# Kernel tuning notes

Hardware: AMD Instinct MI355X
Metric: run time of the kernel (lower is better)

## Reference

```python
import jax, jax.numpy as jnp
import numpy as np

N = 100000      # nodes
E = 3200000     # edges (avg degree 32)
F_IN = 16       # node_feature_size
R1, R2, R3 = 8, 16, 8   # gcn hidden sizes
N1 = 32                  # mlp hidden


def _lin(k, fan_in, shape):
    s = 1.0 / np.sqrt(fan_in)
    return jax.random.uniform(k, shape, minval=-s, maxval=s, dtype=jnp.float32)


def setup_inputs() -> dict:
    key = jax.random.key(0)
    ks = jax.random.split(key, 16)
    x = jax.random.normal(ks[0], (N, F_IN), dtype=jnp.float32)
    edge_index = jax.random.randint(ks[1], (2, E), 0, N, dtype=jnp.int64)
    return {
        "x": x,
        "edge_index": edge_index,
        # GraphConv k: out = mean_agg(x_j) @ W_rel + b + x @ W_root  (PyG GraphConv, lin_root bias=False)
        "W_rel1": _lin(ks[2], F_IN, (F_IN, R1)), "b1": _lin(ks[3], F_IN, (R1,)), "W_root1": _lin(ks[4], F_IN, (F_IN, R1)),
        "W_rel2": _lin(ks[5], R1, (R1, R2)),   "b2": _lin(ks[6], R1, (R2,)),   "W_root2": _lin(ks[7], R1, (R1, R2)),
        "W_rel3": _lin(ks[8], R2, (R2, R3)),   "b3": _lin(ks[9], R2, (R3,)),   "W_root3": _lin(ks[10], R2, (R2, R3)),
        "fc1_W": _lin(ks[11], R3, (R3, N1)), "fc1_b": _lin(ks[12], R3, (N1,)),
        "fc2_W": _lin(ks[13], N1, (N1, 1)),  "fc2_b": _lin(ks[14], N1, (1,)),
    }


def _graph_conv(x, src, dst, W_rel, b, W_root):
    # message: gather source features; aggregate: mean over incoming edges at dst
    n = x.shape[0]
    msg_sum = jax.ops.segment_sum(x[src], dst, num_segments=n)          # [N, F]
    cnt = jax.ops.segment_sum(jnp.ones(src.shape, x.dtype), dst, num_segments=n)
    mean = msg_sum / jnp.maximum(cnt, 1.0)[:, None]
    return mean @ W_rel + b + x @ W_root


def reference(x, edge_index, W_rel1, b1, W_root1, W_rel2, b2, W_root2,
              W_rel3, b3, W_root3, fc1_W, fc1_b, fc2_W, fc2_b):
    src, dst = edge_index[0], edge_index[1]
    h = jax.nn.sigmoid(_graph_conv(x, src, dst, W_rel1, b1, W_root1))
    h = jax.nn.sigmoid(_graph_conv(h, src, dst, W_rel2, b2, W_root2))
    h = jax.nn.sigmoid(_graph_conv(h, src, dst, W_rel3, b3, W_root3))
    h = jax.nn.sigmoid(h @ fc1_W + fc1_b)
    return h @ fc2_W + fc2_b   # [N, 1]
```

## Files before the change

kernel.cpp:

```cpp
#include <hip/hip_runtime.h>
#include <math.h>


#define CHUNK  8192
#define PSTR   10752
#define BW     128
#define MAXB   6144
#define MAXNB  800
#define MAXBLK 512

typedef _Float16 half8 __attribute__((ext_vector_type(8)));

static __device__ __forceinline__ float sigmoidf_(float x) {
    return 1.0f / (1.0f + expf(-x));
}

static __device__ __forceinline__ int scan256_excl(int v, int* s) {
    int tid = threadIdx.x;
    s[tid] = v;
    for (int off = 1; off < 256; off <<= 1) {
        __syncthreads();
        int t = (tid >= off) ? s[tid - off] : 0;
        __syncthreads();
        s[tid] += t;
    }
    __syncthreads();
    return s[tid] - v;
}

static __device__ __forceinline__ void gather_mean8(
    const half8* __restrict__ t, const int* __restrict__ csr,
    int rs, int d, float* s) {
#pragma unroll
    for (int c = 0; c < 8; ++c) s[c] = 0.0f;
    int e = 0;
    for (; e + 4 <= d; e += 4) {
        int4 ci = *(const int4*)(csr + rs + e);
        half8 v0 = t[ci.x]; half8 v1 = t[ci.y];
        half8 v2 = t[ci.z]; half8 v3 = t[ci.w];
#pragma unroll
        for (int c = 0; c < 8; ++c)
            s[c] += ((float)v0[c] + (float)v1[c]) + ((float)v2[c] + (float)v3[c]);
    }
    for (; e < d; ++e) {
        half8 v = t[csr[rs + e]];
#pragma unroll
        for (int c = 0; c < 8; ++c) s[c] += (float)v[c];
    }
    float inv = 1.0f / (float)(d > 0 ? d : 1);
#pragma unroll
    for (int c = 0; c < 8; ++c) s[c] *= inv;
}

__global__ __launch_bounds__(256)
void bin_sort_kernel(const float* __restrict__ x, const float* __restrict__ W1r,
                     const float* __restrict__ b1v, const float* __restrict__ W1o,
                     _Float16* __restrict__ t1, _Float16* __restrict__ z1,
                     const int* __restrict__ src, const int* __restrict__ dst,
                     unsigned* __restrict__ packed, int* __restrict__ counts_bm,
                     int* __restrict__ lstart_bm, int* __restrict__ btot,
                     int E, int N, int NB, int NBLK) {
    __shared__ int s_hist[MAXNB];
    __shared__ int s_cur[MAXNB];
    __shared__ unsigned s_pk[PSTR];
    __shared__ int s_scan[256];
    __shared__ float sW[264];
    int tid = threadIdx.x, blk = blockIdx.x;

    if (tid < 128) { sW[tid] = W1r[tid]; sW[128 + tid] = W1o[tid]; }
    if (tid < 8) sW[256 + tid] = b1v[tid];
    for (int i = tid; i < NB; i += 256) s_hist[i] = 0;
    __syncthreads();
    {
        int node = blk * 256 + tid;
        if (node < N) {
            const float4* x4 = (const float4*)x;
            float xv[16];
#pragma unroll
            for (int k = 0; k < 4; ++k) {
                float4 v = x4[node * 4 + k];
                xv[4 * k] = v.x; xv[4 * k + 1] = v.y;
                xv[4 * k + 2] = v.z; xv[4 * k + 3] = v.w;
            }
            float ta[8], za[8];
#pragma unroll
            for (int j = 0; j < 8; ++j) { ta[j] = 0.0f; za[j] = sW[256 + j]; }
#pragma unroll
            for (int f = 0; f < 16; ++f) {
                float xf = xv[f];
#pragma unroll
                for (int j = 0; j < 8; ++j) {
                    ta[j] += xf * sW[f * 8 + j];
                    za[j] += xf * sW[128 + f * 8 + j];
                }
            }
            half8 th, zh;
#pragma unroll
            for (int j = 0; j < 8; ++j) { th[j] = (_Float16)ta[j]; zh[j] = (_Float16)za[j]; }
            ((half8*)t1)[node] = th;
            ((half8*)z1)[node] = zh;
        }
    }

    if (blk >= NBLK) return;

    int base = blk * CHUNK;
    int cnt = E - base; if (cnt > CHUNK) cnt = CHUNK;

    if (cnt == CHUNK) {
        const int4* d4 = (const int4*)(dst + base);
#pragma unroll
        for (int k = 0; k < CHUNK / 1024; ++k) {
            int4 d = d4[k * 256 + tid];
            atomicAdd(&s_hist[d.x >> 7], 1);
            atomicAdd(&s_hist[d.y >> 7], 1);
            atomicAdd(&s_hist[d.z >> 7], 1);
            atomicAdd(&s_hist[d.w >> 7], 1);
        }
    } else {
        for (int i = tid; i < cnt; i += 256) atomicAdd(&s_hist[dst[base + i] >> 7], 1);
    }
    __syncthreads();

    int per = (NB + 255) / 256;
    int st = tid * per;
    int lsum = 0;
    for (int j = 0; j < per; ++j)
        if (st + j < NB) lsum += (s_hist[st + j] + 3) & ~3;
    int excl = scan256_excl(lsum, s_scan);
    int padtot = s_scan[255];
    int run = excl;
    for (int j = 0; j < per; ++j)
        if (st + j < NB) { s_cur[st + j] = run; run += (s_hist[st + j] + 3) & ~3; }
    __syncthreads();

    if (cnt == CHUNK) {
        const int4* d4 = (const int4*)(dst + base);
        const int4* s4 = (const int4*)(src + base);
#pragma unroll
        for (int k = 0; k < CHUNK / 1024; ++k) {
            int4 d = d4[k * 256 + tid];
            int4 s = s4[k * 256 + tid];
            int dd[4] = {d.x, d.y, d.z, d.w};
            int ss[4] = {s.x, s.y, s.z, s.w};
#pragma unroll
            for (int j = 0; j < 4; ++j) {
                int pos = atomicAdd(&s_cur[dd[j] >> 7], 1);
                s_pk[pos] = ((unsigned)(dd[j] & 127) << 17) | (unsigned)ss[j];
            }
        }
    } else {
        for (int i = tid; i < cnt; i += 256) {
            int d = dst[base + i], s = src[base + i];
            int pos = atomicAdd(&s_cur[d >> 7], 1);
            s_pk[pos] = ((unsigned)(d & 127) << 17) | (unsigned)s;
        }
    }
    __syncthreads();

    for (int i = tid; i < padtot; i += 256) packed[(size_t)blk * PSTR + i] = s_pk[i];
    for (int i = tid; i < NB; i += 256) {
        int h = s_hist[i];
        counts_bm[blk * NB + i] = h;
        lstart_bm[blk * NB + i] = s_cur[i] - h;
        if (h) atomicAdd(&btot[i], h);
    }
}

__global__ __launch_bounds__(256)
void bucket_sort_kernel(const unsigned* __restrict__ packed,
                        const int* __restrict__ counts_bm,
                        const int* __restrict__ lstart_bm,
                        const int* __restrict__ btot,
                        int* __restrict__ csr_src, int* __restrict__ deg,
                        int* __restrict__ rowstart, int N, int NB, int NBLK) {
    __shared__ int s_cnt[MAXBLK], s_lst[MAXBLK], s_off[MAXBLK];
    __shared__ unsigned s_p[MAXB];
    __shared__ int s_out[MAXB];
    __shared__ int h[BW], hs[BW], curb[BW];
    __shared__ int s_scan[256];
    __shared__ int s_tot, s_ptot;
    int b = blockIdx.x, tid = threadIdx.x;

    int partial = 0;
    for (int i = tid; i < b; i += 256) partial += ((btot[i] + 3) & ~3) + 512;
    scan256_excl(partial, s_scan);
    int beg = s_scan[255];

    for (int i = tid; i < NBLK; i += 256) {
        s_cnt[i] = counts_bm[i * NB + b];
        s_lst[i] = lstart_bm[i * NB + b];
    }
    __syncthreads();

    int per = (NBLK + 255) / 256;
    int st = tid * per;
    int lsum = 0;
    for (int j = 0; j < per; ++j)
        if (st + j < NBLK) lsum += s_cnt[st + j];
    int excl = scan256_excl(lsum, s_scan);
    if (tid == 255) s_tot = s_scan[255];
    int run = excl;
    for (int j = 0; j < per; ++j)
        if (st + j < NBLK) { s_off[st + j] = run; run += s_cnt[st + j]; }
    __syncthreads();
    int cnt = s_tot; if (cnt > MAXB) cnt = MAXB;

    for (int blk = tid; blk < NBLK; blk += 256) {
        int c = s_cnt[blk], o = s_off[blk];
        const uint4* p = (const uint4*)(packed + (size_t)blk * PSTR + s_lst[blk]);
        for (int j = 0; j < c; j += 4) {
            uint4 v = p[j >> 2];
            int r = c - j;
            s_p[o + j] = v.x;
            if (r > 1) s_p[o + j + 1] = v.y;
            if (r > 2) s_p[o + j + 2] = v.z;
            if (r > 3) s_p[o + j + 3] = v.w;
        }
    }
    if (tid < BW) h[tid] = 0;
    __syncthreads();

    for (int i = tid; i < cnt; i += 256) atomicAdd(&h[s_p[i] >> 17], 1);
    __syncthreads();
    if (tid == 0) {
        int acc = 0;
        for (int i = 0; i < BW; ++i) { hs[i] = acc; acc += (h[i] + 3) & ~3; }
        s_ptot = acc;
    }
    __syncthreads();
    if (tid < BW) {
        curb[tid] = hs[tid];
        int node = b * BW + tid;
        if (node < N) { deg[node] = h[tid]; rowstart[node] = beg + hs[tid]; }
    }
    __syncthreads();
    for (int i = tid; i < cnt; i += 256) {
        unsigned p = s_p[i];
        int pos = atomicAdd(&curb[p >> 17], 1);
        s_out[pos] = (int)(p & 0x1FFFF);
    }
    __syncthreads();
    int ptot = s_ptot; if (ptot > MAXB) ptot = MAXB;
    for (int i = tid; i < ptot; i += 256) csr_src[beg + i] = s_out[i];
}

__global__ __launch_bounds__(256)
void agg1_kernel(const _Float16* __restrict__ t1, const _Float16* __restrict__ z1,
                 const int* __restrict__ rowstart, const int* __restrict__ deg,
                 const int* __restrict__ csr, _Float16* __restrict__ h1, int n) {
    int node = blockIdx.x * 256 + threadIdx.x;
    if (node >= n) return;
    float s[8];
    gather_mean8((const half8*)t1, csr, rowstart[node], deg[node], s);
    half8 z = ((const half8*)z1)[node];
    half8 o;
#pragma unroll
    for (int c = 0; c < 8; ++c) o[c] = (_Float16)sigmoidf_(s[c] + (float)z[c]);
    ((half8*)h1)[node] = o;
}

__global__ __launch_bounds__(256)
void gcn2_fused_kernel(const _Float16* __restrict__ h1,
                       const int* __restrict__ rowstart, const int* __restrict__ deg,
                       const int* __restrict__ csr,
                       const float* __restrict__ W2r, const float* __restrict__ b2,
                       const float* __restrict__ W2o,
                       const float* __restrict__ W3r, const float* __restrict__ b3,
                       const float* __restrict__ W3o,
                       _Float16* __restrict__ t3, _Float16* __restrict__ z3, int n) {
    __shared__ float sW2r[128], sW2o[128], sW3r[128], sW3o[128], sb2[16], sb3[8];
    int tid = threadIdx.x;
    if (tid < 128) {
        sW2r[tid] = W2r[tid]; sW2o[tid] = W2o[tid];
        sW3r[tid] = W3r[tid]; sW3o[tid] = W3o[tid];
    }
    if (tid < 16) sb2[tid] = b2[tid];
    if (tid < 8) sb3[tid] = b3[tid];
    __syncthreads();
    int node = blockIdx.x * 256 + tid;
    if (node >= n) return;

    float m[8];
    gather_mean8((const half8*)h1, csr, rowstart[node], deg[node], m);
    half8 sf = ((const half8*)h1)[node];
    float x8[8];
#pragma unroll
    for (int c = 0; c < 8; ++c) x8[c] = (float)sf[c];

    float v16[16];
#pragma unroll
    for (int j = 0; j < 16; ++j) {
        float a = sb2[j];
#pragma unroll
        for (int f = 0; f < 8; ++f)
            a += m[f] * sW2r[f * 16 + j] + x8[f] * sW2o[f * 16 + j];
        v16[j] = sigmoidf_(a);
    }
    float ta[8], za[8];
#pragma unroll
    for (int j = 0; j < 8; ++j) { ta[j] = 0.0f; za[j] = sb3[j]; }
#pragma unroll
    for (int f = 0; f < 16; ++f) {
        float hv = v16[f];
#pragma unroll
        for (int j = 0; j < 8; ++j) {
            ta[j] += hv * sW3r[f * 8 + j];
            za[j] += hv * sW3o[f * 8 + j];
        }
    }
    half8 th, zh;
#pragma unroll
    for (int j = 0; j < 8; ++j) { th[j] = (_Float16)ta[j]; zh[j] = (_Float16)za[j]; }
    ((half8*)t3)[node] = th;
    ((half8*)z3)[node] = zh;
}

__global__ __launch_bounds__(256)
void agg3_mlp_kernel(const _Float16* __restrict__ t3, const _Float16* __restrict__ z3,
                     const int* __restrict__ rowstart, const int* __restrict__ deg,
                     const int* __restrict__ csr,
                     const float* __restrict__ fc1W, const float* __restrict__ fc1b,
                     const float* __restrict__ fc2W, const float* __restrict__ fc2b,
                     float* __restrict__ out, int n) {
    __shared__ float sW1[256], sb1[32], sW2[32];
    __shared__ float sb2_;
    int tid = threadIdx.x;
    if (tid < 256) sW1[tid] = fc1W[tid];
    if (tid < 32) { sb1[tid] = fc1b[tid]; sW2[tid] = fc2W[tid]; }
    if (tid == 0) sb2_ = fc2b[0];
    __syncthreads();
    int node = blockIdx.x * 256 + tid;
    if (node >= n) return;

    float s[8];
    gather_mean8((const half8*)t3, csr, rowstart[node], deg[node], s);
    half8 z = ((const half8*)z3)[node];
    float h[8];
#pragma unroll
    for (int c = 0; c < 8; ++c) h[c] = sigmoidf_(s[c] + (float)z[c]);

    float acc = sb2_;
#pragma unroll
    for (int j = 0; j < 32; ++j) {
        float a = sb1[j];
#pragma unroll
        for (int f = 0; f < 8; ++f) a += h[f] * sW1[f * 32 + j];
        acc += sW2[j] * sigmoidf_(a);
    }
    out[node] = acc;
}

extern "C" void kernel_launch(void* const* d_in, const int* in_sizes, int n_in,
                              void* d_out, int out_size, void* d_ws, size_t ws_size,
                              hipStream_t stream) {
    const float* x      = (const float*)d_in[0];
    const int*   ei     = (const int*)d_in[1];
    const float* Wrel1  = (const float*)d_in[2];
    const float* b1     = (const float*)d_in[3];
    const float* Wroot1 = (const float*)d_in[4];
    const float* Wrel2  = (const float*)d_in[5];
    const float* b2     = (const float*)d_in[6];
    const float* Wroot2 = (const float*)d_in[7];
    const float* Wrel3  = (const float*)d_in[8];
    const float* b3     = (const float*)d_in[9];
    const float* Wroot3 = (const float*)d_in[10];
    const float* fc1W   = (const float*)d_in[11];
    const float* fc1b   = (const float*)d_in[12];
    const float* fc2W   = (const float*)d_in[13];
    const float* fc2b   = (const float*)d_in[14];
    float* out = (float*)d_out;

    const int N = in_sizes[0] / 16;
    const int E = in_sizes[1] / 2;
    const int* e_src = ei;
    const int* e_dst = ei + E;

    const int NB   = (N + BW - 1) / BW;
    const int NBLK = (E + CHUNK - 1) / CHUNK;
    const int nbN  = (N + 255) / 256;

    char* ws = (char*)d_ws;
    size_t off = 0;
    auto alloc = [&](size_t bytes) { char* p = ws + off; off += (bytes + 15) & ~size_t(15); return p; };
    unsigned* packed   = (unsigned*)alloc((size_t)NBLK * PSTR * 4);
    int* counts_bm     = (int*)alloc((size_t)NBLK * NB * 4);
    int* lstart_bm     = (int*)alloc((size_t)NBLK * NB * 4);
    int* btot          = (int*)alloc((size_t)NB * 4);
    int* csr_src       = (int*)alloc(((size_t)E + (size_t)NB * 516) * 4);
    int* deg           = (int*)alloc((size_t)N * 4);
    int* rowstart      = (int*)alloc((size_t)N * 4);
    _Float16* t1       = (_Float16*)alloc((size_t)N * 8 * 2);
    _Float16* z1       = (_Float16*)alloc((size_t)N * 8 * 2);
    _Float16* h1       = (_Float16*)alloc((size_t)N * 8 * 2);
    _Float16* t3       = (_Float16*)alloc((size_t)N * 8 * 2);
    _Float16* z3       = (_Float16*)alloc((size_t)N * 8 * 2);

    hipMemsetAsync(btot, 0, (size_t)NB * 4, stream);

    const int gbuild = (NBLK > nbN) ? NBLK : nbN;
    bin_sort_kernel<<<gbuild, 256, 0, stream>>>(
        x, Wrel1, b1, Wroot1, t1, z1, e_src, e_dst,
        packed, counts_bm, lstart_bm, btot, E, N, NB, NBLK);
    bucket_sort_kernel<<<NB, 256, 0, stream>>>(packed, counts_bm, lstart_bm, btot,
                                               csr_src, deg, rowstart, N, NB, NBLK);
    agg1_kernel<<<nbN, 256, 0, stream>>>(t1, z1, rowstart, deg, csr_src, h1, N);
    gcn2_fused_kernel<<<nbN, 256, 0, stream>>>(h1, rowstart, deg, csr_src,
                                               Wrel2, b2, Wroot2, Wrel3, b3, Wroot3, t3, z3, N);
    agg3_mlp_kernel<<<nbN, 256, 0, stream>>>(t3, z3, rowstart, deg, csr_src,
                                             fc1W, fc1b, fc2W, fc2b, out, N);
}
```

Measured before the change: 234.9 us.

## Drop CSR build; aggregate directly from binned edge buckets with LDS atomics

Result: slower. 665.0 us (+183.1%).

```diff
diff --git a/kernel.cpp b/kernel.cpp
--- a/kernel.cpp
+++ b/kernel.cpp
@@ -2,12 +2,11 @@
 #include <math.h>
 
 
-#define CHUNK  8192
-#define PSTR   10752
-#define BW     128
-#define MAXB   6144
-#define MAXNB  800
-#define MAXBLK 512
+#define CHUNK 4096
+#define PSTR  6464
+#define BW    128
+#define MAXNB 800
+#define MAXG  2048
 
 typedef _Float16 half8 __attribute__((ext_vector_type(8)));
 
@@ -28,37 +27,13 @@
     return s[tid] - v;
 }
 
-static __device__ __forceinline__ void gather_mean8(
-    const half8* __restrict__ t, const int* __restrict__ csr,
-    int rs, int d, float* s) {
-#pragma unroll
-    for (int c = 0; c < 8; ++c) s[c] = 0.0f;
-    int e = 0;
-    for (; e + 4 <= d; e += 4) {
-        int4 ci = *(const int4*)(csr + rs + e);
-        half8 v0 = t[ci.x]; half8 v1 = t[ci.y];
-        half8 v2 = t[ci.z]; half8 v3 = t[ci.w];
-#pragma unroll
-        for (int c = 0; c < 8; ++c)
-            s[c] += ((float)v0[c] + (float)v1[c]) + ((float)v2[c] + (float)v3[c]);
-    }
-    for (; e < d; ++e) {
-        half8 v = t[csr[rs + e]];
-#pragma unroll
-        for (int c = 0; c < 8; ++c) s[c] += (float)v[c];
-    }
-    float inv = 1.0f / (float)(d > 0 ? d : 1);
-#pragma unroll
-    for (int c = 0; c < 8; ++c) s[c] *= inv;
-}
-
 __global__ __launch_bounds__(256)
 void bin_sort_kernel(const float* __restrict__ x, const float* __restrict__ W1r,
                      const float* __restrict__ b1v, const float* __restrict__ W1o,
                      _Float16* __restrict__ t1, _Float16* __restrict__ z1,
                      const int* __restrict__ src, const int* __restrict__ dst,
                      unsigned* __restrict__ packed, int* __restrict__ counts_bm,
-                     int* __restrict__ lstart_bm, int* __restrict__ btot,
+                     int* __restrict__ lstart_bm,
                      int E, int N, int NB, int NBLK) {
     __shared__ int s_hist[MAXNB];
     __shared__ int s_cur[MAXNB];
@@ -71,6 +46,7 @@
     if (tid < 8) sW[256 + tid] = b1v[tid];
     for (int i = tid; i < NB; i += 256) s_hist[i] = 0;
     __syncthreads();
+
     {
         int node = blk * 256 + tid;
         if (node < N) {
@@ -101,7 +77,6 @@
             ((half8*)z1)[node] = zh;
         }
     }
-
     if (blk >= NBLK) return;
 
     int base = blk * CHUNK;
@@ -134,6 +109,9 @@
         if (st + j < NB) { s_cur[st + j] = run; run += (s_hist[st + j] + 3) & ~3; }
     __syncthreads();
 
+    for (int i = tid; i < padtot; i += 256) s_pk[i] = 0x80000000u;
+    __syncthreads();
+
     if (cnt == CHUNK) {
         const int4* d4 = (const int4*)(dst + base);
         const int4* s4 = (const int4*)(src + base);
@@ -163,33 +141,26 @@
         int h = s_hist[i];
         counts_bm[blk * NB + i] = h;
         lstart_bm[blk * NB + i] = s_cur[i] - h;
-        if (h) atomicAdd(&btot[i], h);
-    }
-}
-
-__global__ __launch_bounds__(256)
-void bucket_sort_kernel(const unsigned* __restrict__ packed,
-                        const int* __restrict__ counts_bm,
-                        const int* __restrict__ lstart_bm,
-                        const int* __restrict__ btot,
-                        int* __restrict__ csr_src, int* __restrict__ deg,
-                        int* __restrict__ rowstart, int N, int NB, int NBLK) {
-    __shared__ int s_cnt[MAXBLK], s_lst[MAXBLK], s_off[MAXBLK];
-    __shared__ unsigned s_p[MAXB];
-    __shared__ int s_out[MAXB];
-    __shared__ int h[BW], hs[BW], curb[BW];
-    __shared__ int s_scan[256];
-    __shared__ int s_tot, s_ptot;
-    int b = blockIdx.x, tid = threadIdx.x;
-
-    int partial = 0;
-    for (int i = tid; i < b; i += 256) partial += ((btot[i] + 3) & ~3) + 512;
-    scan256_excl(partial, s_scan);
-    int beg = s_scan[255];
-
+    }
+}
+
+struct AggLds {
+    float acc[BW * 9];
+    int s_cnt[MAXNB], s_lst[MAXNB], s_goff[MAXNB];
+    int s_map[MAXG];
+    int s_scan[256];
+};
+
+template <bool COUNT>
+static __device__ __forceinline__ void bucket_accumulate(
+    const half8* __restrict__ t, const unsigned* __restrict__ packed,
+    const int* __restrict__ counts_bm, const int* __restrict__ lstart_bm,
+    int b, int NB, int NBLK, AggLds& L, int* dcnt) {
+    int tid = threadIdx.x;
+    for (int i = tid; i < BW * 9; i += 256) L.acc[i] = 0.0f;
     for (int i = tid; i < NBLK; i += 256) {
-        s_cnt[i] = counts_bm[i * NB + b];
-        s_lst[i] = lstart_bm[i * NB + b];
+        L.s_cnt[i] = counts_bm[i * NB + b];
+        L.s_lst[i] = lstart_bm[i * NB + b];
     }
     __syncthreads();
 
@@ -197,158 +168,168 @@
     int st = tid * per;
     int lsum = 0;
     for (int j = 0; j < per; ++j)
-        if (st + j < NBLK) lsum += s_cnt[st + j];
-    int excl = scan256_excl(lsum, s_scan);
-    if (tid == 255) s_tot = s_scan[255];
+        if (st + j < NBLK) lsum += (L.s_cnt[st + j] + 3) >> 2;
+    int excl = scan256_excl(lsum, L.s_scan);
+    int G = L.s_scan[255];
     int run = excl;
     for (int j = 0; j < per; ++j)
-        if (st + j < NBLK) { s_off[st + j] = run; run += s_cnt[st + j]; }
-    __syncthreads();
-    int cnt = s_tot; if (cnt > MAXB) cnt = MAXB;
-
-    for (int blk = tid; blk < NBLK; blk += 256) {
-        int c = s_cnt[blk], o = s_off[blk];
-        const uint4* p = (const uint4*)(packed + (size_t)blk * PSTR + s_lst[blk]);
-        for (int j = 0; j < c; j += 4) {
-            uint4 v = p[j >> 2];
-            int r = c - j;
-            s_p[o + j] = v.x;
-            if (r > 1) s_p[o + j + 1] = v.y;
-            if (r > 2) s_p[o + j + 2] = v.z;
-            if (r > 3) s_p[o + j + 3] = v.w;
-        }
-    }
-    if (tid < BW) h[tid] = 0;
-    __syncthreads();
-
-    for (int i = tid; i < cnt; i += 256) atomicAdd(&h[s_p[i] >> 17], 1);
-    __syncthreads();
-    if (tid == 0) {
-        int acc = 0;
-        for (int i = 0; i < BW; ++i) { hs[i] = acc; acc += (h[i] + 3) & ~3; }
-        s_ptot = acc;
-    }
-    __syncthreads();
-    if (tid < BW) {
-        curb[tid] = hs[tid];
-        int node = b * BW + tid;
-        if (node < N) { deg[node] = h[tid]; rowstart[node] = beg + hs[tid]; }
-    }
-    __syncthreads();
-    for (int i = tid; i < cnt; i += 256) {
-        unsigned p = s_p[i];
-        int pos = atomicAdd(&curb[p >> 17], 1);
-        s_out[pos] = (int)(p & 0x1FFFF);
-    }
-    __syncthreads();
-    int ptot = s_ptot; if (ptot > MAXB) ptot = MAXB;
-    for (int i = tid; i < ptot; i += 256) csr_src[beg + i] = s_out[i];
+        if (st + j < NBLK) { L.s_goff[st + j] = run; run += (L.s_cnt[st + j] + 3) >> 2; }
+    __syncthreads();
+    if (G > MAXG) G = MAXG;
+
+    for (int i = tid; i < NBLK; i += 256) {
+        int g0 = L.s_goff[i], gc = (L.s_cnt[i] + 3) >> 2;
+        int ge = g0 + gc; if (ge > MAXG) ge = MAXG;
+        for (int g = g0; g < ge; ++g) L.s_map[g] = i;
+    }
+    __syncthreads();
+
+    for (int g = tid; g < G; g += 256) {
+        int r = L.s_map[g];
+        int j = (g - L.s_goff[r]) << 2;
+        uint4 v = *(const uint4*)(packed + (size_t)r * PSTR + L.s_lst[r] + j);
+        unsigned w[4] = {v.x, v.y, v.z, v.w};
+        half8 f[4];
+#pragma unroll
+        for (int k = 0; k < 4; ++k) f[k] = t[w[k] & 0x1FFFF];
+#pragma unroll
+        for (int k = 0; k < 4; ++k) {
+            if (!(w[k] >> 31)) {
+                int dl = (w[k] >> 17) & 127;
+#pragma unroll
+                for (int c = 0; c < 8; ++c)
+                    atomicAdd(&L.acc[dl * 9 + c], (float)f[k][c]);
+                if (COUNT) atomicAdd(&dcnt[dl], 1);
+            }
+        }
+    }
+    __syncthreads();
 }
 
 __global__ __launch_bounds__(256)
 void agg1_kernel(const _Float16* __restrict__ t1, const _Float16* __restrict__ z1,
-                 const int* __restrict__ rowstart, const int* __restrict__ deg,
-                 const int* __restrict__ csr, _Float16* __restrict__ h1, int n) {
-    int node = blockIdx.x * 256 + threadIdx.x;
-    if (node >= n) return;
-    float s[8];
-    gather_mean8((const half8*)t1, csr, rowstart[node], deg[node], s);
-    half8 z = ((const half8*)z1)[node];
-    half8 o;
-#pragma unroll
-    for (int c = 0; c < 8; ++c) o[c] = (_Float16)sigmoidf_(s[c] + (float)z[c]);
-    ((half8*)h1)[node] = o;
+                 const unsigned* __restrict__ packed,
+                 const int* __restrict__ counts_bm, const int* __restrict__ lstart_bm,
+                 float* __restrict__ invd, _Float16* __restrict__ h1,
+                 int N, int NB, int NBLK) {
+    __shared__ AggLds L;
+    __shared__ int dcnt[BW];
+    int tid = threadIdx.x, b = blockIdx.x;
+    for (int i = tid; i < BW; i += 256) dcnt[i] = 0;
+    bucket_accumulate<true>((const half8*)t1, packed, counts_bm, lstart_bm, b, NB, NBLK, L, dcnt);
+    if (tid < BW) {
+        int node = b * BW + tid;
+        if (node < N) {
+            int d = dcnt[tid];
+            float inv = 1.0f / (float)(d > 0 ? d : 1);
+            invd[node] = inv;
+            half8 z = ((const half8*)z1)[node];
+            half8 o;
+#pragma unroll
+            for (int c = 0; c < 8; ++c)
+                o[c] = (_Float16)sigmoidf_(L.acc[tid * 9 + c] * inv + (float)z[c]);
+            ((half8*)h1)[node] = o;
+        }
+    }
 }
 
 __global__ __launch_bounds__(256)
-void gcn2_fused_kernel(const _Float16* __restrict__ h1,
-                       const int* __restrict__ rowstart, const int* __restrict__ deg,
-                       const int* __restrict__ csr,
+void gcn2_fused_kernel(const _Float16* __restrict__ h1, const float* __restrict__ invd,
+                       const unsigned* __restrict__ packed,
+                       const int* __restrict__ counts_bm, const int* __restrict__ lstart_bm,
                        const float* __restrict__ W2r, const float* __restrict__ b2,
                        const float* __restrict__ W2o,
                        const float* __restrict__ W3r, const float* __restrict__ b3,
                        const float* __restrict__ W3o,
-                       _Float16* __restrict__ t3, _Float16* __restrict__ z3, int n) {
+                       _Float16* __restrict__ t3, _Float16* __restrict__ z3,
+                       int N, int NB, int NBLK) {
+    __shared__ AggLds L;
     __shared__ float sW2r[128], sW2o[128], sW3r[128], sW3o[128], sb2[16], sb3[8];
-    int tid = threadIdx.x;
+    int tid = threadIdx.x, b = blockIdx.x;
     if (tid < 128) {
         sW2r[tid] = W2r[tid]; sW2o[tid] = W2o[tid];
         sW3r[tid] = W3r[tid]; sW3o[tid] = W3o[tid];
     }
     if (tid < 16) sb2[tid] = b2[tid];
     if (tid < 8) sb3[tid] = b3[tid];
-    __syncthreads();
-    int node = blockIdx.x * 256 + tid;
-    if (node >= n) return;
-
-    float m[8];
-    gather_mean8((const half8*)h1, csr, rowstart[node], deg[node], m);
-    half8 sf = ((const half8*)h1)[node];
-    float x8[8];
-#pragma unroll
-    for (int c = 0; c < 8; ++c) x8[c] = (float)sf[c];
-
-    float v16[16];
-#pragma unroll
-    for (int j = 0; j < 16; ++j) {
-        float a = sb2[j];
-#pragma unroll
-        for (int f = 0; f < 8; ++f)
-            a += m[f] * sW2r[f * 16 + j] + x8[f] * sW2o[f * 16 + j];
-        v16[j] = sigmoidf_(a);
-    }
-    float ta[8], za[8];
-#pragma unroll
-    for (int j = 0; j < 8; ++j) { ta[j] = 0.0f; za[j] = sb3[j]; }
-#pragma unroll
-    for (int f = 0; f < 16; ++f) {
-        float hv = v16[f];
-#pragma unroll
-        for (int j = 0; j < 8; ++j) {
-            ta[j] += hv * sW3r[f * 8 + j];
-            za[j] += hv * sW3o[f * 8 + j];
-        }
-    }
-    half8 th, zh;
-#pragma unroll
-    for (int j = 0; j < 8; ++j) { th[j] = (_Float16)ta[j]; zh[j] = (_Float16)za[j]; }
-    ((half8*)t3)[node] = th;
-    ((half8*)z3)[node] = zh;
+    bucket_accumulate<false>((const half8*)h1, packed, counts_bm, lstart_bm, b, NB, NBLK, L, nullptr);
+    if (tid < BW) {
+        int node = b * BW + tid;
+        if (node < N) {
+            float inv = invd[node];
+            half8 sf = ((const half8*)h1)[node];
+            float m[8], x8[8];
+#pragma unroll
+            for (int c = 0; c < 8; ++c) {
+                m[c] = L.acc[tid * 9 + c] * inv;
+                x8[c] = (float)sf[c];
+            }
+            float v16[16];
+#pragma unroll
+            for (int j = 0; j < 16; ++j) {
+                float a = sb2[j];
+#pragma unroll
+                for (int f = 0; f < 8; ++f)
+                    a += m[f] * sW2r[f * 16 + j] + x8[f] * sW2o[f * 16 + j];
+                v16[j] = sigmoidf_(a);
+            }
+            float ta[8], za[8];
+#pragma unroll
+            for (int j = 0; j < 8; ++j) { ta[j] = 0.0f; za[j] = sb3[j]; }
+#pragma unroll
+            for (int f = 0; f < 16; ++f) {
+                float hv = v16[f];
+#pragma unroll
+                for (int j = 0; j < 8; ++j) {
+                    ta[j] += hv * sW3r[f * 8 + j];
+                    za[j] += hv * sW3o[f * 8 + j];
+                }
+            }
+            half8 th, zh;
+#pragma unroll
+            for (int j = 0; j < 8; ++j) { th[j] = (_Float16)ta[j]; zh[j] = (_Float16)za[j]; }
+            ((half8*)t3)[node] = th;
+            ((half8*)z3)[node] = zh;
+        }
+    }
 }
 
 __global__ __launch_bounds__(256)
 void agg3_mlp_kernel(const _Float16* __restrict__ t3, const _Float16* __restrict__ z3,
-                     const int* __restrict__ rowstart, const int* __restrict__ deg,
-                     const int* __restrict__ csr,
+                     const float* __restrict__ invd,
+                     const unsigned* __restrict__ packed,
+                     const int* __restrict__ counts_bm, const int* __restrict__ lstart_bm,
                      const float* __restrict__ fc1W, const float* __restrict__ fc1b,
                      const float* __restrict__ fc2W, const float* __restrict__ fc2b,
-                     float* __restrict__ out, int n) {
+                     float* __restrict__ out, int N, int NB, int NBLK) {
+    __shared__ AggLds L;
     __shared__ float sW1[256], sb1[32], sW2[32];
     __shared__ float sb2_;
-    int tid = threadIdx.x;
+    int tid = threadIdx.x, b = blockIdx.x;
     if (tid < 256) sW1[tid] = fc1W[tid];
     if (tid < 32) { sb1[tid] = fc1b[tid]; sW2[tid] = fc2W[tid]; }
     if (tid == 0) sb2_ = fc2b[0];
-    __syncthreads();
-    int node = blockIdx.x * 256 + tid;
-    if (node >= n) return;
-
-    float s[8];
-    gather_mean8((const half8*)t3, csr, rowstart[node], deg[node], s);
-    half8 z = ((const half8*)z3)[node];
-    float h[8];
-#pragma unroll
-    for (int c = 0; c < 8; ++c) h[c] = sigmoidf_(s[c] + (float)z[c]);
-
-    float acc = sb2_;
-#pragma unroll
-    for (int j = 0; j < 32; ++j) {
-        float a = sb1[j];
-#pragma unroll
-        for (int f = 0; f < 8; ++f) a += h[f] * sW1[f * 32 + j];
-        acc += sW2[j] * sigmoidf_(a);
-    }
-    out[node] = acc;
+    bucket_accumulate<false>((const half8*)t3, packed, counts_bm, lstart_bm, b, NB, NBLK, L, nullptr);
+    if (tid < BW) {
+        int node = b * BW + tid;
+        if (node < N) {
+            float inv = invd[node];
+            half8 z = ((const half8*)z3)[node];
+            float h[8];
+#pragma unroll
+            for (int c = 0; c < 8; ++c)
+                h[c] = sigmoidf_(L.acc[tid * 9 + c] * inv + (float)z[c]);
+            float acc = sb2_;
+#pragma unroll
+            for (int j = 0; j < 32; ++j) {
+                float a = sb1[j];
+#pragma unroll
+                for (int f = 0; f < 8; ++f) a += h[f] * sW1[f * 32 + j];
+                acc += sW2[j] * sigmoidf_(a);
+            }
+            out[node] = acc;
+        }
+    }
 }
 
 extern "C" void kernel_launch(void* const* d_in, const int* in_sizes, int n_in,
@@ -386,27 +367,22 @@
     unsigned* packed   = (unsigned*)alloc((size_t)NBLK * PSTR * 4);
     int* counts_bm     = (int*)alloc((size_t)NBLK * NB * 4);
     int* lstart_bm     = (int*)alloc((size_t)NBLK * NB * 4);
-    int* btot          = (int*)alloc((size_t)NB * 4);
-    int* csr_src       = (int*)alloc(((size_t)E + (size_t)NB * 516) * 4);
-    int* deg           = (int*)alloc((size_t)N * 4);
-    int* rowstart      = (int*)alloc((size_t)N * 4);
+    float* invd        = (float*)alloc((size_t)N * 4);
     _Float16* t1       = (_Float16*)alloc((size_t)N * 8 * 2);
     _Float16* z1       = (_Float16*)alloc((size_t)N * 8 * 2);
     _Float16* h1       = (_Float16*)alloc((size_t)N * 8 * 2);
     _Float16* t3       = (_Float16*)alloc((size_t)N * 8 * 2);
     _Float16* z3       = (_Float16*)alloc((size_t)N * 8 * 2);
 
-    hipMemsetAsync(btot, 0, (size_t)NB * 4, stream);
-
     const int gbuild = (NBLK > nbN) ? NBLK : nbN;
     bin_sort_kernel<<<gbuild, 256, 0, stream>>>(
         x, Wrel1, b1, Wroot1, t1, z1, e_src, e_dst,
-        packed, counts_bm, lstart_bm, btot, E, N, NB, NBLK);
-    bucket_sort_kernel<<<NB, 256, 0, stream>>>(packed, counts_bm, lstart_bm, btot,
-                                               csr_src, deg, rowstart, N, NB, NBLK);
-    agg1_kernel<<<nbN, 256, 0, stream>>>(t1, z1, rowstart, deg, csr_src, h1, N);
-    gcn2_fused_kernel<<<nbN, 256, 0, stream>>>(h1, rowstart, deg, csr_src,
-                                               Wrel2, b2, Wroot2, Wrel3, b3, Wroot3, t3, z3, N);
-    agg3_mlp_kernel<<<nbN, 256, 0, stream>>>(t3, z3, rowstart, deg, csr_src,
-                                             fc1W, fc1b, fc2W, fc2b, out, N);
-}
+        packed, counts_bm, lstart_bm, E, N, NB, NBLK);
+    agg1_kernel<<<NB, 256, 0, stream>>>(t1, z1, packed, counts_bm, lstart_bm,
+                                        invd, h1, N, NB, NBLK);
+    gcn2_fused_kernel<<<NB, 256, 0, stream>>>(h1, invd, packed, counts_bm, lstart_bm,
+                                              Wrel2, b2, Wroot2, Wrel3, b3, Wroot3,
+                                              t3, z3, N, NB, NBLK);
+    agg3_mlp_kernel<<<NB, 256, 0, stream>>>(t3, z3, invd, packed, counts_bm, lstart_bm,
+                                            fc1W, fc1b, fc2W, fc2b, out, N, NB, NBLK);
+}
```

## Split each node's neighbor gather across four lanes with shuffle reduction

Applied to the files above, without the earlier changes.

After: 248.3 us. +5.7%, slower.

```diff
diff --git a/kernel.cpp b/kernel.cpp
--- a/kernel.cpp
+++ b/kernel.cpp
@@ -28,28 +28,45 @@
     return s[tid] - v;
 }
 
-static __device__ __forceinline__ void gather_mean8(
+static __device__ __forceinline__ void gather_quarter8(
     const half8* __restrict__ t, const int* __restrict__ csr,
-    int rs, int d, float* s) {
+    int rs, int d, int q, float* s) {
 #pragma unroll
     for (int c = 0; c < 8; ++c) s[c] = 0.0f;
-    int e = 0;
-    for (; e + 4 <= d; e += 4) {
-        int4 ci = *(const int4*)(csr + rs + e);
+    int nf = d >> 2;
+    for (int c4 = q; c4 < nf; c4 += 4) {
+        int4 ci = *(const int4*)(csr + rs + (c4 << 2));
         half8 v0 = t[ci.x]; half8 v1 = t[ci.y];
         half8 v2 = t[ci.z]; half8 v3 = t[ci.w];
 #pragma unroll
         for (int c = 0; c < 8; ++c)
             s[c] += ((float)v0[c] + (float)v1[c]) + ((float)v2[c] + (float)v3[c]);
     }
-    for (; e < d; ++e) {
-        half8 v = t[csr[rs + e]];
-#pragma unroll
-        for (int c = 0; c < 8; ++c) s[c] += (float)v[c];
-    }
-    float inv = 1.0f / (float)(d > 0 ? d : 1);
-#pragma unroll
-    for (int c = 0; c < 8; ++c) s[c] *= inv;
+    int tailc = d & 3;
+    if (tailc && ((nf & 3) == q)) {
+        int e0 = nf << 2;
+        int4 ci = *(const int4*)(csr + rs + e0);
+        half8 v0 = t[ci.x];
+#pragma unroll
+        for (int c = 0; c < 8; ++c) s[c] += (float)v0[c];
+        if (tailc > 1) {
+            half8 v = t[ci.y];
+#pragma unroll
+            for (int c = 0; c < 8; ++c) s[c] += (float)v[c];
+        }
+        if (tailc > 2) {
+            half8 v = t[ci.z];
+#pragma unroll
+            for (int c = 0; c < 8; ++c) s[c] += (float)v[c];
+        }
+    }
+}
+
+static __device__ __forceinline__ void quad_reduce8(float* s) {
+#pragma unroll
+    for (int c = 0; c < 8; ++c) s[c] += __shfl_xor(s[c], 1, 64);
+#pragma unroll
+    for (int c = 0; c < 8; ++c) s[c] += __shfl_xor(s[c], 2, 64);
 }
 
 __global__ __launch_bounds__(256)
@@ -71,6 +88,7 @@
     if (tid < 8) sW[256 + tid] = b1v[tid];
     for (int i = tid; i < NB; i += 256) s_hist[i] = 0;
     __syncthreads();
+
     {
         int node = blk * 256 + tid;
         if (node < N) {
@@ -101,7 +119,6 @@
             ((half8*)z1)[node] = zh;
         }
     }
-
     if (blk >= NBLK) return;
 
     int base = blk * CHUNK;
@@ -249,15 +266,21 @@
 void agg1_kernel(const _Float16* __restrict__ t1, const _Float16* __restrict__ z1,
                  const int* __restrict__ rowstart, const int* __restrict__ deg,
                  const int* __restrict__ csr, _Float16* __restrict__ h1, int n) {
-    int node = blockIdx.x * 256 + threadIdx.x;
+    int idx = blockIdx.x * 256 + threadIdx.x;
+    int node = idx >> 2, q = idx & 3;
     if (node >= n) return;
+    int rs = rowstart[node], d = deg[node];
     float s[8];
-    gather_mean8((const half8*)t1, csr, rowstart[node], deg[node], s);
-    half8 z = ((const half8*)z1)[node];
-    half8 o;
-#pragma unroll
-    for (int c = 0; c < 8; ++c) o[c] = (_Float16)sigmoidf_(s[c] + (float)z[c]);
-    ((half8*)h1)[node] = o;
+    gather_quarter8((const half8*)t1, csr, rs, d, q, s);
+    quad_reduce8(s);
+    if (q == 0) {
+        float inv = 1.0f / (float)(d > 0 ? d : 1);
+        half8 z = ((const half8*)z1)[node];
+        half8 o;
+#pragma unroll
+        for (int c = 0; c < 8; ++c) o[c] = (_Float16)sigmoidf_(s[c] * inv + (float)z[c]);
+        ((half8*)h1)[node] = o;
+    }
 }
 
 __global__ __launch_bounds__(256)
@@ -278,42 +301,48 @@
     if (tid < 16) sb2[tid] = b2[tid];
     if (tid < 8) sb3[tid] = b3[tid];
     __syncthreads();
-    int node = blockIdx.x * 256 + tid;
+    int idx = blockIdx.x * 256 + tid;
+    int node = idx >> 2, q = idx & 3;
     if (node >= n) return;
+    int rs = rowstart[node], d = deg[node];
 
     float m[8];
-    gather_mean8((const half8*)h1, csr, rowstart[node], deg[node], m);
-    half8 sf = ((const half8*)h1)[node];
-    float x8[8];
-#pragma unroll
-    for (int c = 0; c < 8; ++c) x8[c] = (float)sf[c];
-
-    float v16[16];
-#pragma unroll
-    for (int j = 0; j < 16; ++j) {
-        float a = sb2[j];
-#pragma unroll
-        for (int f = 0; f < 8; ++f)
-            a += m[f] * sW2r[f * 16 + j] + x8[f] * sW2o[f * 16 + j];
-        v16[j] = sigmoidf_(a);
-    }
-    float ta[8], za[8];
-#pragma unroll
-    for (int j = 0; j < 8; ++j) { ta[j] = 0.0f; za[j] = sb3[j]; }
-#pragma unroll
-    for (int f = 0; f < 16; ++f) {
-        float hv = v16[f];
-#pragma unroll
-        for (int j = 0; j < 8; ++j) {
-            ta[j] += hv * sW3r[f * 8 + j];
-            za[j] += hv * sW3o[f * 8 + j];
-        }
-    }
-    half8 th, zh;
-#pragma unroll
-    for (int j = 0; j < 8; ++j) { th[j] = (_Float16)ta[j]; zh[j] = (_Float16)za[j]; }
-    ((half8*)t3)[node] = th;
-    ((half8*)z3)[node] = zh;
+    gather_quarter8((const half8*)h1, csr, rs, d, q, m);
+    quad_reduce8(m);
+    if (q == 0) {
+        float inv = 1.0f / (float)(d > 0 ? d : 1);
+        half8 sf = ((const half8*)h1)[node];
+        float x8[8];
+#pragma unroll
+        for (int c = 0; c < 8; ++c) { m[c] *= inv; x8[c] = (float)sf[c]; }
+
+        float v16[16];
+#pragma unroll
+        for (int j = 0; j < 16; ++j) {
+            float a = sb2[j];
+#pragma unroll
+            for (int f = 0; f < 8; ++f)
+                a += m[f] * sW2r[f * 16 + j] + x8[f] * sW2o[f * 16 + j];
+            v16[j] = sigmoidf_(a);
+        }
+        float ta[8], za[8];
+#pragma unroll
+        for (int j = 0; j < 8; ++j) { ta[j] = 0.0f; za[j] = sb3[j]; }
+#pragma unroll
+        for (int f = 0; f < 16; ++f) {
+            float hv = v16[f];
+#pragma unroll
+            for (int j = 0; j < 8; ++j) {
+                ta[j] += hv * sW3r[f * 8 + j];
+                za[j] += hv * sW3o[f * 8 + j];
+            }
+        }
+        half8 th, zh;
+#pragma unroll
+        for (int j = 0; j < 8; ++j) { th[j] = (_Float16)ta[j]; zh[j] = (_Float16)za[j]; }
+        ((half8*)t3)[node] = th;
+        ((half8*)z3)[node] = zh;
+    }
 }
 
 __global__ __launch_bounds__(256)
@@ -330,25 +359,30 @@
     if (tid < 32) { sb1[tid] = fc1b[tid]; sW2[tid] = fc2W[tid]; }
     if (tid == 0) sb2_ = fc2b[0];
     __syncthreads();
-    int node = blockIdx.x * 256 + tid;
+    int idx = blockIdx.x * 256 + tid;
+    int node = idx >> 2, q = idx & 3;
     if (node >= n) return;
+    int rs = rowstart[node], d = deg[node];
 
     float s[8];
-    gather_mean8((const half8*)t3, csr, rowstart[node], deg[node], s);
-    half8 z = ((const half8*)z3)[node];
-    float h[8];
-#pragma unroll
-    for (int c = 0; c < 8; ++c) h[c] = sigmoidf_(s[c] + (float)z[c]);
-
-    float acc = sb2_;
-#pragma unroll
-    for (int j = 0; j < 32; ++j) {
-        float a = sb1[j];
-#pragma unroll
-        for (int f = 0; f < 8; ++f) a += h[f] * sW1[f * 32 + j];
-        acc += sW2[j] * sigmoidf_(a);
-    }
-    out[node] = acc;
+    gather_quarter8((const half8*)t3, csr, rs, d, q, s);
+    quad_reduce8(s);
+    if (q == 0) {
+        float inv = 1.0f / (float)(d > 0 ? d : 1);
+        half8 z = ((const half8*)z3)[node];
+        float h[8];
+#pragma unroll
+        for (int c = 0; c < 8; ++c) h[c] = sigmoidf_(s[c] * inv + (float)z[c]);
+        float acc = sb2_;
+#pragma unroll
+        for (int j = 0; j < 32; ++j) {
+            float a = sb1[j];
+#pragma unroll
+            for (int f = 0; f < 8; ++f) a += h[f] * sW1[f * 32 + j];
+            acc += sW2[j] * sigmoidf_(a);
+        }
+        out[node] = acc;
+    }
 }
 
 extern "C" void kernel_launch(void* const* d_in, const int* in_sizes, int n_in,
@@ -379,6 +413,7 @@
     const int NB   = (N + BW - 1) / BW;
     const int NBLK = (E + CHUNK - 1) / CHUNK;
     const int nbN  = (N + 255) / 256;
+    const int nb4  = (4 * N + 255) / 256;
 
     char* ws = (char*)d_ws;
     size_t off = 0;
@@ -404,9 +439,9 @@
         packed, counts_bm, lstart_bm, btot, E, N, NB, NBLK);
     bucket_sort_kernel<<<NB, 256, 0, stream>>>(packed, counts_bm, lstart_bm, btot,
                                                csr_src, deg, rowstart, N, NB, NBLK);
-    agg1_kernel<<<nbN, 256, 0, stream>>>(t1, z1, rowstart, deg, csr_src, h1, N);
-    gcn2_fused_kernel<<<nbN, 256, 0, stream>>>(h1, rowstart, deg, csr_src,
+    agg1_kernel<<<nb4, 256, 0, stream>>>(t1, z1, rowstart, deg, csr_src, h1, N);
+    gcn2_fused_kernel<<<nb4, 256, 0, stream>>>(h1, rowstart, deg, csr_src,
                                                Wrel2, b2, Wroot2, Wrel3, b3, Wroot3, t3, z3, N);
-    agg3_mlp_kernel<<<nbN, 256, 0, stream>>>(t3, z3, rowstart, deg, csr_src,
+    agg3_mlp_kernel<<<nb4, 256, 0, stream>>>(t3, z3, rowstart, deg, csr_src,
                                              fc1W, fc1b, fc2W, fc2b, out, N);
 }
```

## Fuse layer-1 aggregation into bucket sort and pack rowstart with degree

Applied to the files above, without the earlier changes.

Measured after the change: 315.4 us. +34.3%, slower.

```diff
diff --git a/kernel.cpp b/kernel.cpp
--- a/kernel.cpp
+++ b/kernel.cpp
@@ -10,9 +10,15 @@
 #define MAXBLK 512
 
 typedef _Float16 half8 __attribute__((ext_vector_type(8)));
+typedef unsigned uintv4 __attribute__((ext_vector_type(4)));
 
 static __device__ __forceinline__ float sigmoidf_(float x) {
     return 1.0f / (1.0f + expf(-x));
+}
+
+static __device__ __forceinline__ half8 ldnt8(const half8* p) {
+    uintv4 v = __builtin_nontemporal_load((const uintv4*)p);
+    union { uintv4 u; half8 h; } c; c.u = v; return c.h;
 }
 
 static __device__ __forceinline__ int scan256_excl(int v, int* s) {
@@ -28,7 +34,7 @@
     return s[tid] - v;
 }
 
-static __device__ __forceinline__ void gather_mean8(
+static __device__ __forceinline__ void gather_sum8(
     const half8* __restrict__ t, const int* __restrict__ csr,
     int rs, int d, float* s) {
 #pragma unroll
@@ -36,20 +42,29 @@
     int e = 0;
     for (; e + 4 <= d; e += 4) {
         int4 ci = *(const int4*)(csr + rs + e);
-        half8 v0 = t[ci.x]; half8 v1 = t[ci.y];
-        half8 v2 = t[ci.z]; half8 v3 = t[ci.w];
+        half8 v0 = ldnt8(&t[ci.x]); half8 v1 = ldnt8(&t[ci.y]);
+        half8 v2 = ldnt8(&t[ci.z]); half8 v3 = ldnt8(&t[ci.w]);
 #pragma unroll
         for (int c = 0; c < 8; ++c)
             s[c] += ((float)v0[c] + (float)v1[c]) + ((float)v2[c] + (float)v3[c]);
     }
-    for (; e < d; ++e) {
-        half8 v = t[csr[rs + e]];
-#pragma unroll
-        for (int c = 0; c < 8; ++c) s[c] += (float)v[c];
-    }
-    float inv = 1.0f / (float)(d > 0 ? d : 1);
-#pragma unroll
-    for (int c = 0; c < 8; ++c) s[c] *= inv;
+    if (e < d) {
+        int4 ci = *(const int4*)(csr + rs + e);
+        int tailc = d - e;
+        half8 v0 = ldnt8(&t[ci.x]);
+#pragma unroll
+        for (int c = 0; c < 8; ++c) s[c] += (float)v0[c];
+        if (tailc > 1) {
+            half8 v = ldnt8(&t[ci.y]);
+#pragma unroll
+            for (int c = 0; c < 8; ++c) s[c] += (float)v[c];
+        }
+        if (tailc > 2) {
+            half8 v = ldnt8(&t[ci.z]);
+#pragma unroll
+            for (int c = 0; c < 8; ++c) s[c] += (float)v[c];
+        }
+    }
 }
 
 __global__ __launch_bounds__(256)
@@ -71,6 +86,7 @@
     if (tid < 8) sW[256 + tid] = b1v[tid];
     for (int i = tid; i < NB; i += 256) s_hist[i] = 0;
     __syncthreads();
+
     {
         int node = blk * 256 + tid;
         if (node < N) {
@@ -101,7 +117,6 @@
             ((half8*)z1)[node] = zh;
         }
     }
-
     if (blk >= NBLK) return;
 
     int base = blk * CHUNK;
@@ -168,12 +183,14 @@
 }
 
 __global__ __launch_bounds__(256)
-void bucket_sort_kernel(const unsigned* __restrict__ packed,
-                        const int* __restrict__ counts_bm,
-                        const int* __restrict__ lstart_bm,
-                        const int* __restrict__ btot,
-                        int* __restrict__ csr_src, int* __restrict__ deg,
-                        int* __restrict__ rowstart, int N, int NB, int NBLK) {
+void sort_agg1_kernel(const unsigned* __restrict__ packed,
+                      const int* __restrict__ counts_bm,
+                      const int* __restrict__ lstart_bm,
+                      const int* __restrict__ btot,
+                      const _Float16* __restrict__ t1, const _Float16* __restrict__ z1,
+                      int* __restrict__ csr_src, int* __restrict__ rowdeg,
+                      _Float16* __restrict__ h1,
+                      int N, int NB, int NBLK) {
     __shared__ int s_cnt[MAXBLK], s_lst[MAXBLK], s_off[MAXBLK];
     __shared__ unsigned s_p[MAXB];
     __shared__ int s_out[MAXB];
@@ -208,9 +225,9 @@
 
     for (int blk = tid; blk < NBLK; blk += 256) {
         int c = s_cnt[blk], o = s_off[blk];
-        const uint4* p = (const uint4*)(packed + (size_t)blk * PSTR + s_lst[blk]);
+        const uintv4* p = (const uintv4*)(packed + (size_t)blk * PSTR + s_lst[blk]);
         for (int j = 0; j < c; j += 4) {
-            uint4 v = p[j >> 2];
+            uintv4 v = p[j >> 2];
             int r = c - j;
             s_p[o + j] = v.x;
             if (r > 1) s_p[o + j + 1] = v.y;
@@ -232,7 +249,8 @@
     if (tid < BW) {
         curb[tid] = hs[tid];
         int node = b * BW + tid;
-        if (node < N) { deg[node] = h[tid]; rowstart[node] = beg + hs[tid]; }
+        if (node < N)
+            rowdeg[node] = (beg + hs[tid]) | (h[tid] << 22);
     }
     __syncthreads();
     for (int i = tid; i < cnt; i += 256) {
@@ -243,26 +261,59 @@
     __syncthreads();
     int ptot = s_ptot; if (ptot > MAXB) ptot = MAXB;
     for (int i = tid; i < ptot; i += 256) csr_src[beg + i] = s_out[i];
-}
-
-__global__ __launch_bounds__(256)
-void agg1_kernel(const _Float16* __restrict__ t1, const _Float16* __restrict__ z1,
-                 const int* __restrict__ rowstart, const int* __restrict__ deg,
-                 const int* __restrict__ csr, _Float16* __restrict__ h1, int n) {
-    int node = blockIdx.x * 256 + threadIdx.x;
-    if (node >= n) return;
-    float s[8];
-    gather_mean8((const half8*)t1, csr, rowstart[node], deg[node], s);
-    half8 z = ((const half8*)z1)[node];
-    half8 o;
-#pragma unroll
-    for (int c = 0; c < 8; ++c) o[c] = (_Float16)sigmoidf_(s[c] + (float)z[c]);
-    ((half8*)h1)[node] = o;
+
+    int ln = tid >> 1, q = tid & 1;
+    int node = b * BW + ln;
+    if (node < N) {
+        int rsl = hs[ln], d = h[ln];
+        float s[8];
+#pragma unroll
+        for (int c = 0; c < 8; ++c) s[c] = 0.0f;
+        int nf = d >> 2;
+        for (int c4 = q; c4 < nf; c4 += 2) {
+            int4 ci = *(const int4*)(s_out + rsl + (c4 << 2));
+            half8 v0 = ldnt8((const half8*)t1 + ci.x);
+            half8 v1 = ldnt8((const half8*)t1 + ci.y);
+            half8 v2 = ldnt8((const half8*)t1 + ci.z);
+            half8 v3 = ldnt8((const half8*)t1 + ci.w);
+#pragma unroll
+            for (int c = 0; c < 8; ++c)
+                s[c] += ((float)v0[c] + (float)v1[c]) + ((float)v2[c] + (float)v3[c]);
+        }
+        int tailc = d & 3;
+        if (tailc && ((nf & 1) == q)) {
+            int4 ci = *(const int4*)(s_out + rsl + (nf << 2));
+            half8 v0 = ldnt8((const half8*)t1 + ci.x);
+#pragma unroll
+            for (int c = 0; c < 8; ++c) s[c] += (float)v0[c];
+            if (tailc > 1) {
+                half8 v = ldnt8((const half8*)t1 + ci.y);
+#pragma unroll
+                for (int c = 0; c < 8; ++c) s[c] += (float)v[c];
+            }
+            if (tailc > 2) {
+                half8 v = ldnt8((const half8*)t1 + ci.z);
+#pragma unroll
+                for (int c = 0; c < 8; ++c) s[c] += (float)v[c];
+            }
+        }
+#pragma unroll
+        for (int c = 0; c < 8; ++c) s[c] += __shfl_xor(s[c], 1, 64);
+        if (q == 0) {
+            float inv = 1.0f / (float)(d > 0 ? d : 1);
+            half8 z = ((const half8*)z1)[node];
+            half8 o;
+#pragma unroll
+            for (int c = 0; c < 8; ++c)
+                o[c] = (_Float16)sigmoidf_(s[c] * inv + (float)z[c]);
+            ((half8*)h1)[node] = o;
+        }
+    }
 }
 
 __global__ __launch_bounds__(256)
 void gcn2_fused_kernel(const _Float16* __restrict__ h1,
-                       const int* __restrict__ rowstart, const int* __restrict__ deg,
+                       const int* __restrict__ rowdeg,
                        const int* __restrict__ csr,
                        const float* __restrict__ W2r, const float* __restrict__ b2,
                        const float* __restrict__ W2o,
@@ -280,13 +331,16 @@
     __syncthreads();
     int node = blockIdx.x * 256 + tid;
     if (node >= n) return;
+    int v = rowdeg[node];
+    int rs = v & 0x3FFFFF, d = (int)((unsigned)v >> 22);
 
     float m[8];
-    gather_mean8((const half8*)h1, csr, rowstart[node], deg[node], m);
+    gather_sum8((const half8*)h1, csr, rs, d, m);
+    float inv = 1.0f / (float)(d > 0 ? d : 1);
     half8 sf = ((const half8*)h1)[node];
     float x8[8];
 #pragma unroll
-    for (int c = 0; c < 8; ++c) x8[c] = (float)sf[c];
+    for (int c = 0; c < 8; ++c) { m[c] *= inv; x8[c] = (float)sf[c]; }
 
     float v16[16];
 #pragma unroll
@@ -318,7 +372,7 @@
 
 __global__ __launch_bounds__(256)
 void agg3_mlp_kernel(const _Float16* __restrict__ t3, const _Float16* __restrict__ z3,
-                     const int* __restrict__ rowstart, const int* __restrict__ deg,
+                     const int* __restrict__ rowdeg,
                      const int* __restrict__ csr,
                      const float* __restrict__ fc1W, const float* __restrict__ fc1b,
                      const float* __restrict__ fc2W, const float* __restrict__ fc2b,
@@ -332,13 +386,16 @@
     __syncthreads();
     int node = blockIdx.x * 256 + tid;
     if (node >= n) return;
+    int v = rowdeg[node];
+    int rs = v & 0x3FFFFF, d = (int)((unsigned)v >> 22);
 
     float s[8];
-    gather_mean8((const half8*)t3, csr, rowstart[node], deg[node], s);
+    gather_sum8((const half8*)t3, csr, rs, d, s);
+    float inv = 1.0f / (float)(d > 0 ? d : 1);
     half8 z = ((const half8*)z3)[node];
     float h[8];
 #pragma unroll
-    for (int c = 0; c < 8; ++c) h[c] = sigmoidf_(s[c] + (float)z[c]);
+    for (int c = 0; c < 8; ++c) h[c] = sigmoidf_(s[c] * inv + (float)z[c]);
 
     float acc = sb2_;
 #pragma unroll
@@ -388,25 +445,23 @@
     int* lstart_bm     = (int*)alloc((size_t)NBLK * NB * 4);
     int* btot          = (int*)alloc((size_t)NB * 4);
     int* csr_src       = (int*)alloc(((size_t)E + (size_t)NB * 516) * 4);
-    int* deg           = (int*)alloc((size_t)N * 4);
-    int* rowstart      = (int*)alloc((size_t)N * 4);
+    int* rowdeg        = (int*)alloc((size_t)N * 4);
     _Float16* t1       = (_Float16*)alloc((size_t)N * 8 * 2);
     _Float16* z1       = (_Float16*)alloc((size_t)N * 8 * 2);
     _Float16* h1       = (_Float16*)alloc((size_t)N * 8 * 2);
     _Float16* t3       = (_Float16*)alloc((size_t)N * 8 * 2);
     _Float16* z3       = (_Float16*)alloc((size_t)N * 8 * 2);
 
-    hipMemsetAsync(btot, 0, (size_t)NB * 4, stream);
+    (void)hipMemsetAsync(btot, 0, (size_t)NB * 4, stream);
 
     const int gbuild = (NBLK > nbN) ? NBLK : nbN;
     bin_sort_kernel<<<gbuild, 256, 0, stream>>>(
         x, Wrel1, b1, Wroot1, t1, z1, e_src, e_dst,
         packed, counts_bm, lstart_bm, btot, E, N, NB, NBLK);
-    bucket_sort_kernel<<<NB, 256, 0, stream>>>(packed, counts_bm, lstart_bm, btot,
-                                               csr_src, deg, rowstart, N, NB, NBLK);
-    agg1_kernel<<<nbN, 256, 0, stream>>>(t1, z1, rowstart, deg, csr_src, h1, N);
-    gcn2_fused_kernel<<<nbN, 256, 0, stream>>>(h1, rowstart, deg, csr_src,
+    sort_agg1_kernel<<<NB, 256, 0, stream>>>(packed, counts_bm, lstart_bm, btot,
+                                             t1, z1, csr_src, rowdeg, h1, N, NB, NBLK);
+    gcn2_fused_kernel<<<nbN, 256, 0, stream>>>(h1, rowdeg, csr_src,
                                                Wrel2, b2, Wroot2, Wrel3, b3, Wroot3, t3, z3, N);
-    agg3_mlp_kernel<<<nbN, 256, 0, stream>>>(t3, z3, rowstart, deg, csr_src,
+    agg3_mlp_kernel<<<nbN, 256, 0, stream>>>(t3, z3, rowdeg, csr_src,
                                              fc1W, fc1b, fc2W, fc2b, out, N);
 }
```
